# Kernel optimization log

Hardware: AMD Instinct MI355X
Metric: run time of the kernel (lower is better)

The kernel has to match this reference:

```python
import jax, jax.numpy as jnp
import numpy as np
import math

D_MODEL = 1024
N_HEADS = 16
D_HEAD = D_MODEL // N_HEADS
D_FF = 4 * D_MODEL
EPS = 1e-5


def layer_norm(x, gamma, beta):
    mu = jnp.mean(x, axis=-1, keepdims=True)
    var = jnp.var(x, axis=-1, keepdims=True)
    return (x - mu) * jax.lax.rsqrt(var + EPS) * gamma + beta


def setup_inputs() -> dict:
    key = jax.random.key(0)
    ks = jax.random.split(key, 8)
    B, C, D = 32, 256, D_MODEL
    s = 0.02
    return {
        "X": jax.random.normal(ks[0], (B, C, D), dtype=jnp.float32),
        "W_qkv": jax.random.normal(ks[1], (D, 3 * D), dtype=jnp.float32) * s,
        "b_qkv": jnp.zeros((3 * D,), dtype=jnp.float32),
        "W_proj": jax.random.normal(ks[2], (D, D), dtype=jnp.float32) * s,
        "b_proj": jnp.zeros((D,), dtype=jnp.float32),
        "g1": jnp.ones((D,), dtype=jnp.float32),
        "beta1": jnp.zeros((D,), dtype=jnp.float32),
        "g2": jnp.ones((D,), dtype=jnp.float32),
        "beta2": jnp.zeros((D,), dtype=jnp.float32),
        "W_ff1": jax.random.normal(ks[3], (D, D_FF), dtype=jnp.float32) * s,
        "b_ff1": jnp.zeros((D_FF,), dtype=jnp.float32),
        "W_ff2": jax.random.normal(ks[4], (D_FF, D), dtype=jnp.float32) * s,
        "b_ff2": jnp.zeros((D,), dtype=jnp.float32),
    }


def reference(X, W_qkv, b_qkv, W_proj, b_proj, g1, beta1, g2, beta2,
              W_ff1, b_ff1, W_ff2, b_ff2):
    B, C, D = X.shape
    H, Dh = N_HEADS, D_HEAD
    scale = 1.0 / math.sqrt(Dh)

    Xn = layer_norm(X, g1, beta1)
    qkv = Xn @ W_qkv + b_qkv                       # [B, C, 3D]
    q, k, v = jnp.split(qkv, 3, axis=-1)
    # split heads -> [B, H, C, Dh]
    sh = lambda t: t.reshape(B, C, H, Dh).transpose(0, 2, 1, 3)
    q, k, v = sh(q), sh(k), sh(v)

    scores = jnp.einsum("bhcd,bhkd->bhck", q, k) * scale  # [B, H, C, C]
    attn = jax.nn.softmax(scores, axis=-1)
    ctx = jnp.einsum("bhck,bhkd->bhcd", attn, v)           # [B, H, C, Dh]
    ctx = ctx.transpose(0, 2, 1, 3).reshape(B, C, D)

    X1 = X + (ctx @ W_proj + b_proj)
    X2n = layer_norm(X1, g2, beta2)
    h = jax.nn.gelu(X2n @ W_ff1 + b_ff1, approximate=False)
    X_out = X1 + (h @ W_ff2 + b_ff2)
    A = attn.mean(axis=1)                                   # [B, C, C]
    return (X_out, A)
```

## Files before the change

### kernel.cpp

```cpp
#include <hip/hip_runtime.h>
#include <cstdint>
#include <cstddef>

typedef short bf16x8 __attribute__((ext_vector_type(8)));
typedef float f32x4 __attribute__((ext_vector_type(4)));
typedef unsigned short u16;
typedef u16 u16x8 __attribute__((ext_vector_type(8)));

#define GLD16(gptr, lptr)                                                            \
  __builtin_amdgcn_global_load_lds((const __attribute__((address_space(1))) void*)(gptr), \
                                   (__attribute__((address_space(3))) void*)(lptr), 16, 0, 0)

__device__ __forceinline__ u16 f2bf(float f) {
  union { float f; unsigned u; } v; v.f = f;
  unsigned r = v.u + 0x7FFF + ((v.u >> 16) & 1);
  return (u16)(r >> 16);
}
__device__ __forceinline__ float bf2f(u16 h) {
  union { unsigned u; float f; } v; v.u = ((unsigned)h) << 16;
  return v.f;
}

__device__ __forceinline__ bf16x8 lds_read_sw64(const u16* base, int row, int col) {
  int byt = row * 128 + col * 2;
  byt ^= (row & 7) << 4;
  return *(const bf16x8*)((const char*)base + byt);
}

__global__ __launch_bounds__(256) void transpose_cast(const float* __restrict__ in,
                                                      u16* __restrict__ out, int R, int C) {
  __shared__ float tile[32][33];
  const int tx = threadIdx.x, ty = threadIdx.y;
  const int c0 = blockIdx.x * 32, r0 = blockIdx.y * 32;
#pragma unroll
  for (int i = 0; i < 32; i += 8)
    tile[ty + i][tx] = in[(size_t)(r0 + ty + i) * C + c0 + tx];
  __syncthreads();
#pragma unroll
  for (int i = 0; i < 32; i += 8)
    out[(size_t)(c0 + ty + i) * R + r0 + tx] = f2bf(tile[tx][ty + i]);
}

__global__ __launch_bounds__(256) void layernorm_bf16(const float* __restrict__ X,
                                                      const float* __restrict__ g,
                                                      const float* __restrict__ be,
                                                      u16* __restrict__ out) {
  const int row = blockIdx.x, t = threadIdx.x;
  const int lane = t & 63, wave = t >> 6;
  const float* x = X + (size_t)row * 1024;
  __shared__ float part[4];
  float v[4]; float s = 0.f;
#pragma unroll
  for (int i = 0; i < 4; ++i) { v[i] = x[t + i * 256]; s += v[i]; }
#pragma unroll
  for (int o = 32; o >= 1; o >>= 1) s += __shfl_xor(s, o);
  if (lane == 0) part[wave] = s;
  __syncthreads();
  const float mu = (part[0] + part[1] + part[2] + part[3]) * (1.f / 1024.f);
  float d2 = 0.f;
#pragma unroll
  for (int i = 0; i < 4; ++i) { float d = v[i] - mu; d2 += d * d; }
#pragma unroll
  for (int o = 32; o >= 1; o >>= 1) d2 += __shfl_xor(d2, o);
  __syncthreads();
  if (lane == 0) part[wave] = d2;
  __syncthreads();
  const float var = (part[0] + part[1] + part[2] + part[3]) * (1.f / 1024.f);
  const float rstd = rsqrtf(var + 1e-5f);
#pragma unroll
  for (int i = 0; i < 4; ++i) {
    const int c = t + i * 256;
    out[(size_t)row * 1024 + c] = f2bf((v[i] - mu) * rstd * g[c] + be[c]);
  }
}

template <int EPI>
__global__ __launch_bounds__(256) void gemm_bf16(const u16* __restrict__ A,
                                                 const u16* __restrict__ Bt,
                                                 const float* __restrict__ bias,
                                                 const float* __restrict__ res,
                                                 float* __restrict__ outf,
                                                 u16* __restrict__ outb,
                                                 int M, int N, int K) {
  __shared__ u16 As[128 * 64];
  __shared__ u16 Bs[128 * 64];
  const int t = threadIdx.x, lane = t & 63, wave = t >> 6;
  const int bm = blockIdx.y * 128, bn = blockIdx.x * 128;
  const int wm = (wave >> 1) * 64, wn = (wave & 1) * 64;
  f32x4 acc[4][4] = {};

  int srow[4], scol[4];
#pragma unroll
  for (int is = 0; is < 4; ++is) {
    int L = (is * 2048 + t * 8) * 2;
    int x = (L ^ ((L >> 3) & 0x70)) >> 1;
    srow[is] = x >> 6; scol[is] = x & 63;
  }

  for (int kt = 0; kt < K; kt += 64) {
#pragma unroll
    for (int is = 0; is < 4; ++is) {
      const u16* gp = A + (size_t)(bm + srow[is]) * K + kt + scol[is];
      GLD16(gp, (char*)As + is * 4096 + wave * 1024);
    }
#pragma unroll
    for (int is = 0; is < 4; ++is) {
      const u16* gp = Bt + (size_t)(bn + srow[is]) * K + kt + scol[is];
      GLD16(gp, (char*)Bs + is * 4096 + wave * 1024);
    }
    __syncthreads();
#pragma unroll
    for (int ks = 0; ks < 2; ++ks) {
      bf16x8 af[4], bfr[4];
#pragma unroll
      for (int m = 0; m < 4; ++m)
        af[m] = lds_read_sw64(As, wm + m * 16 + (lane & 15), ks * 32 + (lane >> 4) * 8);
#pragma unroll
      for (int n = 0; n < 4; ++n)
        bfr[n] = lds_read_sw64(Bs, wn + n * 16 + (lane & 15), ks * 32 + (lane >> 4) * 8);
#pragma unroll
      for (int m = 0; m < 4; ++m)
#pragma unroll
        for (int n = 0; n < 4; ++n)
          acc[m][n] = __builtin_amdgcn_mfma_f32_16x16x32_bf16(af[m], bfr[n], acc[m][n], 0, 0, 0);
    }
    __syncthreads();
  }

  const int r0 = (lane >> 4) * 4, cc = lane & 15;
#pragma unroll
  for (int m = 0; m < 4; ++m) {
#pragma unroll
    for (int n = 0; n < 4; ++n) {
      const int col = bn + wn + n * 16 + cc;
      const float bv = bias[col];
#pragma unroll
      for (int r = 0; r < 4; ++r) {
        const int row = bm + wm + m * 16 + r0 + r;
        const float v = acc[m][n][r] + bv;
        const size_t o = (size_t)row * N + col;
        if (EPI == 0) {
          outb[o] = f2bf(v);
        } else if (EPI == 1) {
          outf[o] = res[o] + v;
        } else {
          const float gl = 0.5f * v * (1.0f + erff(v * 0.70710678118654752f));
          outb[o] = f2bf(gl);
        }
      }
    }
  }
}

__global__ __launch_bounds__(256) void attn_scores(const u16* __restrict__ qkv,
                                                   u16* __restrict__ probs) {
  __shared__ u16 Ks[256 * 64];
  __shared__ u16 Qs[64 * 64];
  const int t = threadIdx.x, lane = t & 63, wave = t >> 6;
  const int qb = blockIdx.x * 64, h = blockIdx.y, b = blockIdx.z;
  const size_t row0 = (size_t)b * 256 * 3072;

#pragma unroll
  for (int is = 0; is < 8; ++is) {
    int L = (is * 2048 + t * 8) * 2;
    int x = (L ^ ((L >> 3) & 0x70)) >> 1;
    int kk = x >> 6, d = x & 63;
    const u16* gp = qkv + row0 + (size_t)kk * 3072 + 1024 + h * 64 + d;
    GLD16(gp, (char*)Ks + is * 4096 + wave * 1024);
  }
#pragma unroll
  for (int is = 0; is < 2; ++is) {
    int L = (is * 2048 + t * 8) * 2;
    int x = (L ^ ((L >> 3) & 0x70)) >> 1;
    int q = x >> 6, d = x & 63;
    const u16* gp = qkv + row0 + (size_t)(qb + q) * 3072 + h * 64 + d;
    GLD16(gp, (char*)Qs + is * 4096 + wave * 1024);
  }
  __syncthreads();

  f32x4 acc[16] = {};
  bf16x8 aq[2];
#pragma unroll
  for (int ks = 0; ks < 2; ++ks)
    aq[ks] = lds_read_sw64(Qs, wave * 16 + (lane & 15), ks * 32 + (lane >> 4) * 8);
#pragma unroll
  for (int nf = 0; nf < 16; ++nf) {
#pragma unroll
    for (int ks = 0; ks < 2; ++ks) {
      bf16x8 bk = lds_read_sw64(Ks, nf * 16 + (lane & 15), ks * 32 + (lane >> 4) * 8);
      acc[nf] = __builtin_amdgcn_mfma_f32_16x16x32_bf16(aq[ks], bk, acc[nf], 0, 0, 0);
    }
  }

  const int r0 = (lane >> 4) * 4, cc = lane & 15;
  const float sc = 0.125f;
#pragma unroll
  for (int r = 0; r < 4; ++r) {
    float mx = -1e30f;
#pragma unroll
    for (int nf = 0; nf < 16; ++nf) mx = fmaxf(mx, acc[nf][r]);
#pragma unroll
    for (int o = 8; o >= 1; o >>= 1) mx = fmaxf(mx, __shfl_xor(mx, o));
    float s = 0.f;
#pragma unroll
    for (int nf = 0; nf < 16; ++nf) {
      float e = __expf((acc[nf][r] - mx) * sc);
      acc[nf][r] = e; s += e;
    }
#pragma unroll
    for (int o = 8; o >= 1; o >>= 1) s += __shfl_xor(s, o);
    const float rinv = 1.f / s;
    const int qrow = qb + wave * 16 + r0 + r;
    u16* prow = probs + (size_t)((b * 16 + h) * 256 + qrow) * 256;
#pragma unroll
    for (int nf = 0; nf < 16; ++nf)
      prow[nf * 16 + cc] = f2bf(acc[nf][r] * rinv);
  }
}

__global__ __launch_bounds__(256) void amean(const u16* __restrict__ probs,
                                             float* __restrict__ A) {
  const int bq = blockIdx.x;
  const int b = bq >> 8, q = bq & 255;
  const int t = threadIdx.x;
  float s = 0.f;
#pragma unroll
  for (int h = 0; h < 16; ++h)
    s += bf2f(probs[(size_t)((b * 16 + h) * 256 + q) * 256 + t]);
  A[(size_t)bq * 256 + t] = s * (1.f / 16.f);
}

__global__ __launch_bounds__(256) void attn_pv(const u16* __restrict__ qkv,
                                               const u16* __restrict__ probs,
                                               u16* __restrict__ ctx) {
  __shared__ u16 Vs[64 * 256];
  const int t = threadIdx.x, lane = t & 63, wave = t >> 6;
  const int h = blockIdx.x, b = blockIdx.y;

#pragma unroll
  for (int p = 0; p < 8; ++p) {
    int idx = p * 2048 + t * 8;
    int kk = idx >> 6, d0 = idx & 63;
    u16x8 vv = *(const u16x8*)(qkv + (size_t)(b * 256 + kk) * 3072 + 2048 + h * 64 + d0);
#pragma unroll
    for (int j = 0; j < 8; ++j) {
      int d = d0 + j;
      int byt = (d * 512 + kk * 2) ^ ((d & 7) << 4);
      *(u16*)((char*)Vs + byt) = vv[j];
    }
  }
  __syncthreads();

  f32x4 acc[4][4] = {};
  const u16* Pb = probs + (size_t)((b * 16 + h) * 256) * 256;
  const int cc = lane & 15, kg = (lane >> 4) * 8;
#pragma unroll
  for (int kt = 0; kt < 8; ++kt) {
    bf16x8 a[4], v[4];
#pragma unroll
    for (int m = 0; m < 4; ++m)
      a[m] = *(const bf16x8*)(Pb + (size_t)(wave * 64 + m * 16 + cc) * 256 + kt * 32 + kg);
#pragma unroll
    for (int n = 0; n < 4; ++n) {
      int d = n * 16 + cc;
      int kk = kt * 32 + kg;
      int byt = (d * 512 + kk * 2) ^ ((d & 7) << 4);
      v[n] = *(const bf16x8*)((const char*)Vs + byt);
    }
#pragma unroll
    for (int m = 0; m < 4; ++m)
#pragma unroll
      for (int n = 0; n < 4; ++n)
        acc[m][n] = __builtin_amdgcn_mfma_f32_16x16x32_bf16(a[m], v[n], acc[m][n], 0, 0, 0);
  }

  const int r0 = (lane >> 4) * 4;
#pragma unroll
  for (int m = 0; m < 4; ++m) {
    const int q = wave * 64 + m * 16 + r0;
#pragma unroll
    for (int n = 0; n < 4; ++n) {
      const int col = h * 64 + n * 16 + cc;
#pragma unroll
      for (int r = 0; r < 4; ++r)
        ctx[(size_t)(b * 256 + q + r) * 1024 + col] = f2bf(acc[m][n][r]);
    }
  }
}

extern "C" void kernel_launch(void* const* d_in, const int* in_sizes, int n_in,
                              void* d_out, int out_size, void* d_ws, size_t ws_size,
                              hipStream_t stream) {
  const float* X      = (const float*)d_in[0];
  const float* W_qkv  = (const float*)d_in[1];
  const float* b_qkv  = (const float*)d_in[2];
  const float* W_proj = (const float*)d_in[3];
  const float* b_proj = (const float*)d_in[4];
  const float* g1     = (const float*)d_in[5];
  const float* beta1  = (const float*)d_in[6];
  const float* g2     = (const float*)d_in[7];
  const float* beta2  = (const float*)d_in[8];
  const float* W_ff1  = (const float*)d_in[9];
  const float* b_ff1  = (const float*)d_in[10];
  const float* W_ff2  = (const float*)d_in[11];
  const float* b_ff2  = (const float*)d_in[12];

  float* Xout = (float*)d_out;
  float* Aout = (float*)d_out + 8388608;

  char* ws = (char*)d_ws;
  const size_t MB = 1u << 20;
  u16* xn    = (u16*)(ws + 0);
  u16* wqkv  = (u16*)(ws + 16 * MB);
  u16* wproj = (u16*)(ws + 22 * MB);
  u16* wff1  = (u16*)(ws + 24 * MB);
  u16* wff2  = (u16*)(ws + 32 * MB);
  u16* qkv   = (u16*)(ws + 40 * MB);
  u16* probs = (u16*)(ws + 88 * MB);
  u16* hbuf  = probs;
  float* x1  = (float*)(ws + 152 * MB);
  u16* ctx   = xn;
  u16* x1n   = xn;

  const dim3 tb(32, 8);
  transpose_cast<<<dim3(96, 32),  tb, 0, stream>>>(W_qkv,  wqkv, 1024, 3072);
  transpose_cast<<<dim3(32, 32),  tb, 0, stream>>>(W_proj, wproj, 1024, 1024);
  transpose_cast<<<dim3(128, 32), tb, 0, stream>>>(W_ff1,  wff1, 1024, 4096);
  transpose_cast<<<dim3(32, 128), tb, 0, stream>>>(W_ff2,  wff2, 4096, 1024);

  layernorm_bf16<<<8192, 256, 0, stream>>>(X, g1, beta1, xn);

  gemm_bf16<0><<<dim3(24, 64), 256, 0, stream>>>(xn, wqkv, b_qkv, nullptr, nullptr, qkv,
                                                 8192, 3072, 1024);

  attn_scores<<<dim3(4, 16, 32), 256, 0, stream>>>(qkv, probs);
  amean<<<8192, 256, 0, stream>>>(probs, Aout);
  attn_pv<<<dim3(16, 32), 256, 0, stream>>>(qkv, probs, ctx);

  gemm_bf16<1><<<dim3(8, 64), 256, 0, stream>>>(ctx, wproj, b_proj, X, x1, nullptr,
                                                8192, 1024, 1024);

  layernorm_bf16<<<8192, 256, 0, stream>>>(x1, g2, beta2, x1n);

  gemm_bf16<2><<<dim3(32, 64), 256, 0, stream>>>(x1n, wff1, b_ff1, nullptr, nullptr, hbuf,
                                                 8192, 4096, 1024);

  gemm_bf16<1><<<dim3(8, 64), 256, 0, stream>>>(hbuf, wff2, b_ff2, x1, Xout, nullptr,
                                                8192, 1024, 4096);
}
```

Measured before the change: 396.4 us.

## Replace GEMM with 4-stage pipelined 512-thread kernel, larger tiles, tanh GELU

Replaces the single-buffered 128x128 GEMM with a templated kernel that keeps a 4-deep ring of K=32 LDS stages. It issues async global-to-LDS loads three stages ahead and uses explicit vmcnt waits with one barrier per step. It also uses 512-thread blocks with larger 256x128 or 256x256 tiles, a swizzled block-index mapping for L2 locality, and setprio around MFMA. The FF1 epilogue swaps exact erf GELU for a tanh approximation, which changes numerics slightly.

```diff
diff --git a/kernel.cpp b/kernel.cpp
--- a/kernel.cpp
+++ b/kernel.cpp
@@ -19,6 +19,14 @@
 __device__ __forceinline__ float bf2f(u16 h) {
   union { unsigned u; float f; } v; v.u = ((unsigned)h) << 16;
   return v.f;
+}
+
+template <int N> __device__ __forceinline__ void vmwait() {
+  if constexpr (N == 0) asm volatile("s_waitcnt vmcnt(0)" ::: "memory");
+  else if constexpr (N == 3) asm volatile("s_waitcnt vmcnt(3)" ::: "memory");
+  else if constexpr (N == 4) asm volatile("s_waitcnt vmcnt(4)" ::: "memory");
+  else if constexpr (N == 6) asm volatile("s_waitcnt vmcnt(6)" ::: "memory");
+  else asm volatile("s_waitcnt vmcnt(8)" ::: "memory");
 }
 
 __device__ __forceinline__ bf16x8 lds_read_sw64(const u16* base, int row, int col) {
@@ -74,69 +82,94 @@
   }
 }
 
-template <int EPI>
-__global__ __launch_bounds__(256) void gemm_bf16(const u16* __restrict__ A,
-                                                 const u16* __restrict__ Bt,
-                                                 const float* __restrict__ bias,
-                                                 const float* __restrict__ res,
-                                                 float* __restrict__ outf,
-                                                 u16* __restrict__ outb,
-                                                 int M, int N, int K) {
-  __shared__ u16 As[128 * 64];
-  __shared__ u16 Bs[128 * 64];
+template <int EPI, int WM, int WN, int MF, int NF>
+__global__ __launch_bounds__(512, 2) void gemm_pipe(const u16* __restrict__ A,
+                                                    const u16* __restrict__ Bt,
+                                                    const float* __restrict__ bias,
+                                                    const float* __restrict__ res,
+                                                    float* __restrict__ outf,
+                                                    u16* __restrict__ outb,
+                                                    int M, int N, int K) {
+  constexpr int BM = WM * MF * 16, BN = WN * NF * 16;
+  constexpr int LA = BM / 128, LB = BN / 128, L = LA + LB;
+  constexpr int ASZ = BM * 32, BSZ = BN * 32;
+  __shared__ u16 lds[4 * (ASZ + BSZ)];
+
   const int t = threadIdx.x, lane = t & 63, wave = t >> 6;
-  const int bm = blockIdx.y * 128, bn = blockIdx.x * 128;
-  const int wm = (wave >> 1) * 64, wn = (wave & 1) * 64;
-  f32x4 acc[4][4] = {};
-
-  int srow[4], scol[4];
-#pragma unroll
-  for (int is = 0; is < 4; ++is) {
-    int L = (is * 2048 + t * 8) * 2;
-    int x = (L ^ ((L >> 3) & 0x70)) >> 1;
-    srow[is] = x >> 6; scol[is] = x & 63;
-  }
-
-  for (int kt = 0; kt < K; kt += 64) {
-#pragma unroll
-    for (int is = 0; is < 4; ++is) {
-      const u16* gp = A + (size_t)(bm + srow[is]) * K + kt + scol[is];
-      GLD16(gp, (char*)As + is * 4096 + wave * 1024);
-    }
-#pragma unroll
-    for (int is = 0; is < 4; ++is) {
-      const u16* gp = Bt + (size_t)(bn + srow[is]) * K + kt + scol[is];
-      GLD16(gp, (char*)Bs + is * 4096 + wave * 1024);
-    }
-    __syncthreads();
-#pragma unroll
-    for (int ks = 0; ks < 2; ++ks) {
-      bf16x8 af[4], bfr[4];
-#pragma unroll
-      for (int m = 0; m < 4; ++m)
-        af[m] = lds_read_sw64(As, wm + m * 16 + (lane & 15), ks * 32 + (lane >> 4) * 8);
-#pragma unroll
-      for (int n = 0; n < 4; ++n)
-        bfr[n] = lds_read_sw64(Bs, wn + n * 16 + (lane & 15), ks * 32 + (lane >> 4) * 8);
-#pragma unroll
-      for (int m = 0; m < 4; ++m)
-#pragma unroll
-        for (int n = 0; n < 4; ++n)
-          acc[m][n] = __builtin_amdgcn_mfma_f32_16x16x32_bf16(af[m], bfr[n], acc[m][n], 0, 0, 0);
-    }
-    __syncthreads();
-  }
-
-  const int r0 = (lane >> 4) * 4, cc = lane & 15;
-#pragma unroll
-  for (int m = 0; m < 4; ++m) {
-#pragma unroll
-    for (int n = 0; n < 4; ++n) {
-      const int col = bn + wn + n * 16 + cc;
+  const int wm = wave / WN, wn = wave % WN;
+  const int l15 = lane & 15, l16 = lane >> 4;
+
+  const int lb = (blockIdx.x & 7) * ((int)gridDim.x >> 3) + ((int)blockIdx.x >> 3);
+  const int NBN = N / BN;
+  const int bm = (lb / NBN) * BM, bn = (lb % NBN) * BN;
+
+  const u16* asrcj[LA];
+  const u16* bsrcj[LB];
+#pragma unroll
+  for (int j = 0; j < LA; ++j)
+    asrcj[j] = A + (size_t)(bm + j * 128 + (t >> 2)) * K + (t & 3) * 8;
+#pragma unroll
+  for (int j = 0; j < LB; ++j)
+    bsrcj[j] = Bt + (size_t)(bn + j * 128 + (t >> 2)) * K + (t & 3) * 8;
+
+  auto stage = [&](int p) {
+    const int koff = p * 32;
+    char* abase = (char*)lds + (p & 3) * (ASZ * 2) + wave * 1024;
+    char* bbase = (char*)lds + 8 * ASZ + (p & 3) * (BSZ * 2) + wave * 1024;
+#pragma unroll
+    for (int j = 0; j < LA; ++j) GLD16(asrcj[j] + koff, abase + j * 8192);
+#pragma unroll
+    for (int j = 0; j < LB; ++j) GLD16(bsrcj[j] + koff, bbase + j * 8192);
+  };
+
+  int aoff[MF], boff[NF];
+#pragma unroll
+  for (int m = 0; m < MF; ++m) aoff[m] = (wm * MF * 16 + m * 16 + l15) * 32 + l16 * 8;
+#pragma unroll
+  for (int n = 0; n < NF; ++n) boff[n] = (wn * NF * 16 + n * 16 + l15) * 32 + l16 * 8;
+
+  const int nkt = K >> 5;
+#pragma unroll
+  for (int p = 0; p < 3; ++p) stage(p);
+
+  f32x4 acc[MF][NF] = {};
+
+#pragma unroll 1
+  for (int kt = 0; kt < nkt; ++kt) {
+    const int rem = nkt - 1 - kt;
+    if (rem >= 2) vmwait<2 * L>();
+    else if (rem == 1) vmwait<L>();
+    else vmwait<0>();
+    __builtin_amdgcn_s_barrier();
+    __builtin_amdgcn_sched_barrier(0);
+    if (rem >= 3) stage(kt + 3);
+
+    const u16* ab = lds + (kt & 3) * ASZ;
+    const u16* bb = lds + 4 * ASZ + (kt & 3) * BSZ;
+    bf16x8 a[MF], b[NF];
+#pragma unroll
+    for (int m = 0; m < MF; ++m) a[m] = *(const bf16x8*)(ab + aoff[m]);
+#pragma unroll
+    for (int n = 0; n < NF; ++n) b[n] = *(const bf16x8*)(bb + boff[n]);
+    __builtin_amdgcn_s_setprio(1);
+#pragma unroll
+    for (int m = 0; m < MF; ++m)
+#pragma unroll
+      for (int n = 0; n < NF; ++n)
+        acc[m][n] = __builtin_amdgcn_mfma_f32_16x16x32_bf16(a[m], b[n], acc[m][n], 0, 0, 0);
+    __builtin_amdgcn_s_setprio(0);
+  }
+
+  const int r0 = l16 * 4;
+#pragma unroll
+  for (int m = 0; m < MF; ++m) {
+#pragma unroll
+    for (int n = 0; n < NF; ++n) {
+      const int col = bn + wn * NF * 16 + n * 16 + l15;
       const float bv = bias[col];
 #pragma unroll
       for (int r = 0; r < 4; ++r) {
-        const int row = bm + wm + m * 16 + r0 + r;
+        const int row = bm + wm * MF * 16 + m * 16 + r0 + r;
         const float v = acc[m][n][r] + bv;
         const size_t o = (size_t)row * N + col;
         if (EPI == 0) {
@@ -144,8 +177,10 @@
         } else if (EPI == 1) {
           outf[o] = res[o] + v;
         } else {
-          const float gl = 0.5f * v * (1.0f + erff(v * 0.70710678118654752f));
-          outb[o] = f2bf(gl);
+          const float u = 0.7978845608f * (v + 0.044715f * v * v * v);
+          const float e = __expf(2.f * u);
+          const float th = 1.f - 2.f / (1.f + e);
+          outb[o] = f2bf(0.5f * v * (1.f + th));
         }
       }
     }
@@ -330,21 +365,21 @@
 
   layernorm_bf16<<<8192, 256, 0, stream>>>(X, g1, beta1, xn);
 
-  gemm_bf16<0><<<dim3(24, 64), 256, 0, stream>>>(xn, wqkv, b_qkv, nullptr, nullptr, qkv,
-                                                 8192, 3072, 1024);
+  gemm_pipe<0, 4, 2, 4, 4><<<768, 512, 0, stream>>>(xn, wqkv, b_qkv, nullptr, nullptr, qkv,
+                                                    8192, 3072, 1024);
 
   attn_scores<<<dim3(4, 16, 32), 256, 0, stream>>>(qkv, probs);
   amean<<<8192, 256, 0, stream>>>(probs, Aout);
   attn_pv<<<dim3(16, 32), 256, 0, stream>>>(qkv, probs, ctx);
 
-  gemm_bf16<1><<<dim3(8, 64), 256, 0, stream>>>(ctx, wproj, b_proj, X, x1, nullptr,
-                                                8192, 1024, 1024);
+  gemm_pipe<1, 4, 2, 4, 4><<<256, 512, 0, stream>>>(ctx, wproj, b_proj, X, x1, nullptr,
+                                                    8192, 1024, 1024);
 
   layernorm_bf16<<<8192, 256, 0, stream>>>(x1, g2, beta2, x1n);
 
-  gemm_bf16<2><<<dim3(32, 64), 256, 0, stream>>>(x1n, wff1, b_ff1, nullptr, nullptr, hbuf,
-                                                 8192, 4096, 1024);
-
-  gemm_bf16<1><<<dim3(8, 64), 256, 0, stream>>>(hbuf, wff2, b_ff2, x1, Xout, nullptr,
-                                                8192, 1024, 4096);
-}
+  gemm_pipe<2, 2, 4, 8, 4><<<512, 512, 0, stream>>>(x1n, wff1, b_ff1, nullptr, nullptr, hbuf,
+                                                    8192, 4096, 1024);
+
+  gemm_pipe<1, 4, 2, 4, 4><<<256, 512, 0, stream>>>(hbuf, wff2, b_ff2, x1, Xout, nullptr,
+                                                    8192, 1024, 4096);
+}
```

Result: faster. 380.3 us (-4.1%).
